# Kernel optimization log

Hardware: AMD Instinct MI355X
Metric: run time of the kernel (lower is better)

## Reference

```python
import jax, jax.numpy as jnp
import numpy as np
from jax import lax

EPS = 1e-5

def _conv(x, w, pad):
    # x: NCHW, w: OIHW, stride 1
    return lax.conv_general_dilated(x, w, (1, 1), [(pad, pad), (pad, pad)],
                                    dimension_numbers=('NCHW', 'OIHW', 'NCHW'))

def _binconv(x, w):
    # IR-Net/ReActNet HardBinaryConv: sign-binarized weights scaled by per-filter
    # mean |w| (alpha), sign-binarized activations; clip-based STE for backward.
    alpha = jnp.mean(jnp.abs(w), axis=(1, 2, 3), keepdims=True)  # [O,1,1,1]
    wc = jnp.clip(w, -1.0, 1.0)
    bw = lax.stop_gradient(alpha * jnp.sign(w) - wc) + wc
    xc = jnp.clip(x, -1.0, 1.0)
    ba = lax.stop_gradient(jnp.sign(x) - xc) + xc
    return _conv(ba, bw, 1)

def _bn(x, g, b, m, v):
    # inference-mode BatchNorm2d with running stats
    inv = g / jnp.sqrt(v + EPS)
    return x * inv[None, :, None, None] + (b - m * inv)[None, :, None, None]

def _pool(x):
    return lax.reduce_window(x, -jnp.inf, lax.max, (1, 1, 2, 2), (1, 1, 2, 2), 'VALID')

def _htanh(x):
    return jnp.clip(x, -1.0, 1.0)

def setup_inputs() -> dict:
    key = jax.random.key(0)
    ks = jax.random.split(key, 40)
    B = 256
    d = {'x': jax.random.normal(ks[0], (B, 3, 32, 32), jnp.float32)}
    shapes = [(128, 3, 3, 3), (128, 128, 3, 3), (256, 128, 3, 3),
              (256, 256, 3, 3), (512, 256, 3, 3), (512, 512, 3, 3)]
    chans = [128, 128, 256, 256, 512, 512]
    ki = 1
    for i, (ws, c) in enumerate(zip(shapes, chans)):
        fan_in = ws[1] * 9
        d[f'w{i}'] = jax.random.normal(ks[ki], ws, jnp.float32) / np.sqrt(fan_in); ki += 1
        d[f'g{i}'] = jnp.ones((c,), jnp.float32)
        d[f'b{i}'] = jnp.zeros((c,), jnp.float32)
        d[f'm{i}'] = jax.random.normal(ks[ki], (c,), jnp.float32) * 0.1; ki += 1
        d[f'v{i}'] = jax.random.uniform(ks[ki], (c,), jnp.float32, 0.5, 1.5); ki += 1
    d['fcw'] = jax.random.normal(ks[ki], (10, 512 * 4 * 4), jnp.float32) * 0.01
    d['fcb'] = jnp.zeros((10,), jnp.float32)
    return d

def reference(x, w0, g0, b0, m0, v0, w1, g1, b1, m1, v1, w2, g2, b2, m2, v2,
              w3, g3, b3, m3, v3, w4, g4, b4, m4, v4, w5, g5, b5, m5, v5,
              fcw, fcb):
    h = _bn(_conv(x, w0, 1), g0, b0, m0, v0)            # [B,128,32,32]
    h = _htanh(_bn(_pool(_binconv(h, w1)), g1, b1, m1, v1))   # [B,128,16,16]
    h = _htanh(_bn(_binconv(h, w2), g2, b2, m2, v2))          # [B,256,16,16]
    h = _htanh(_bn(_pool(_binconv(h, w3)), g3, b3, m3, v3))   # [B,256,8,8]
    h = _htanh(_bn(_binconv(h, w4), g4, b4, m4, v4))          # [B,512,8,8]
    h = _htanh(_bn(_pool(_binconv(h, w5)), g5, b5, m5, v5))   # [B,512,4,4]
    h = h.reshape(h.shape[0], -1)                             # [B,8192]
    return h @ fcw.T + fcb                                    # [B,10]
```

## Files before the change

kernel.cpp:

```cpp
#include <hip/hip_runtime.h>
#include <cstdint>

#define EPS 1e-5
typedef unsigned long long u64;
typedef unsigned int u32;

struct BnArgs { const float *g[6], *b[6], *m[6], *v[6]; };
struct PackArgs { const float* w[5]; u64* wb[5]; };

__global__ void bn_prep_all(BnArgs p, double* __restrict__ scale_all,
                            double* __restrict__ shift_all) {
    int i = blockIdx.x * 256 + threadIdx.x;
    if (i >= 1792) return;
    int l, base;
    if (i < 128)       { l = 0; base = 0; }
    else if (i < 256)  { l = 1; base = 128; }
    else if (i < 512)  { l = 2; base = 256; }
    else if (i < 768)  { l = 3; base = 512; }
    else if (i < 1280) { l = 4; base = 768; }
    else               { l = 5; base = 1280; }
    const int c = i - base;
    double inv = (double)p.g[l][c] / sqrt((double)p.v[l][c] + EPS);
    scale_all[i] = inv;
    shift_all[i] = (double)p.b[l][c] - (double)p.m[l][c] * inv;
}

__global__ void zero_out(float* __restrict__ out, int n) {
    int i = blockIdx.x * blockDim.x + threadIdx.x;
    if (i < n) out[i] = 0.f;
}

__global__ void pack_all(PackArgs pk, const double* __restrict__ scale_all,
                         double* __restrict__ A_all) {
    const int ob = blockIdx.x;
    const int t = threadIdx.x;
    int l, base, Cin, bnoff;
    if (ob < 128)       { l = 0; base = 0;    Cin = 128; bnoff = 128; }
    else if (ob < 384)  { l = 1; base = 128;  Cin = 128; bnoff = 256; }
    else if (ob < 640)  { l = 2; base = 384;  Cin = 256; bnoff = 512; }
    else if (ob < 1152) { l = 3; base = 640;  Cin = 256; bnoff = 768; }
    else                { l = 4; base = 1152; Cin = 512; bnoff = 1280; }
    const int o = ob - base;
    const float* wo = pk.w[l] + (size_t)o * Cin * 9;

    double s = 0.0;
    for (int k = t; k < Cin * 9; k += 256) s += fabs((double)wo[k]);
    __shared__ double red[256];
    red[t] = s;
    __syncthreads();
    for (int r = 128; r > 0; r >>= 1) {
        if (t < r) red[t] += red[t + r];
        __syncthreads();
    }
    if (t == 0) {
        double alpha = red[0] / (double)(Cin * 9);
        A_all[ob] = alpha * scale_all[bnoff + o];
    }

    const int W64 = Cin / 64;
    u64* wb = pk.wb[l];
    for (int e = t; e < 9 * W64; e += 256) {
        int tap = e / W64, word = e % W64;
        u64 bits = 0;
        for (int j = 0; j < 64; ++j) {
            int c = word * 64 + j;
            if (wo[c * 9 + tap] < 0.f) bits |= (1ull << j);
        }
        wb[((size_t)o * 9 + tap) * W64 + word] = bits;
    }
}

__global__ __launch_bounds__(256) void conv0_pack(
        const float* __restrict__ x, const float* __restrict__ w0,
        const double* __restrict__ scale, const double* __restrict__ shift,
        u64* __restrict__ bits0) {
    __shared__ double wlds[128 * 27];
    __shared__ double sc[128], sh[128];
    const int tid = threadIdx.x;
    for (int e = tid; e < 128 * 27; e += 256) wlds[e] = (double)w0[e];
    for (int e = tid; e < 128; e += 256) { sc[e] = scale[e]; sh[e] = shift[e]; }
    __syncthreads();

    const int n = blockIdx.y;
    const int p = blockIdx.x * 256 + tid;
    const int y = p >> 5, xx = p & 31;
    const float* xn = x + (size_t)n * 3 * 32 * 32;

    double win[27];
#pragma unroll
    for (int c = 0; c < 3; ++c)
#pragma unroll
        for (int dy = 0; dy < 3; ++dy)
#pragma unroll
            for (int dx = 0; dx < 3; ++dx) {
                const int yy = y + dy - 1, xs = xx + dx - 1;
                const bool ok = (yy >= 0 && yy < 32 && xs >= 0 && xs < 32);
                win[(c * 3 + dy) * 3 + dx] = ok ? (double)xn[(c * 32 + yy) * 32 + xs] : 0.0;
            }

    u64* op = bits0 + ((size_t)n * 1024 + p) * 2;
#pragma unroll
    for (int og = 0; og < 2; ++og) {
        u64 word = 0;
#pragma unroll 2
        for (int j = 0; j < 64; ++j) {
            const int o = og * 64 + j;
            const double* wo = &wlds[o * 27];
            double acc = 0.0;
#pragma unroll
            for (int k = 0; k < 27; ++k) acc = fma(wo[k], win[k], acc);
            const double val = acc * sc[o] + sh[o];
            word |= (u64)(val < 0.0) << j;
        }
        op[og] = word;
    }
}

template<int H, int W, int W64, int OTOT, int OPW, int MINW>
__global__ __launch_bounds__(256, MINW) void bconv_np(
        const u64* __restrict__ in_bits, const u64* __restrict__ wb,
        const double* __restrict__ A, const double* __restrict__ B,
        u32* __restrict__ out_bits) {
    const int tid = threadIdx.x;
    const int wave = tid >> 6, lane = tid & 63;
    constexpr int WPI = (H * W) / 64;
    constexpr int IPB = (WPI >= 4) ? 1 : 4 / WPI;
    const int img = (IPB == 1) ? blockIdx.y : blockIdx.y * IPB + wave;
    const int pw  = (IPB == 1) ? wave : 0;
    const int p = pw * 64 + lane;
    const int y = p / W, x = p % W;
    const int obase = blockIdx.x * OPW;

    __shared__ u64 wlds[OPW * 9 * W64];
    __shared__ double Alds[OPW], Blds[OPW];
    {
        const u64* wg = wb + (size_t)obase * 9 * W64;
        for (int e = tid; e < OPW * 9 * W64; e += 256) wlds[e] = wg[e];
        for (int e = tid; e < OPW; e += 256) { Alds[e] = A[obase + e]; Blds[e] = B[obase + e]; }
    }
    __syncthreads();

    const u64* ib = in_bits + (size_t)img * H * W * W64;
    u64 win[3][3][W64];
    bool tv[3][3];
    int nvalid = 0;
#pragma unroll
    for (int dy = 0; dy < 3; ++dy)
#pragma unroll
        for (int dx = 0; dx < 3; ++dx) {
            const int yy = y + dy - 1, xs = x + dx - 1;
            const bool ok = (yy >= 0 && yy < H && xs >= 0 && xs < W);
            tv[dy][dx] = ok;
            nvalid += ok ? 1 : 0;
            const u64* q = ib + ((size_t)yy * W + xs) * W64;
#pragma unroll
            for (int k = 0; k < W64; ++k) win[dy][dx][k] = ok ? q[k] : 0ull;
        }
    const int basev = nvalid * 64 * W64;

    u32 obuf[OPW / 32];
    u32 cur = 0;
    for (int oc = 0; oc < OPW; ++oc) {
        const u64* wo = &wlds[oc * 9 * W64];
        int pop = 0;
#pragma unroll
        for (int dy = 0; dy < 3; ++dy)
#pragma unroll
            for (int dx = 0; dx < 3; ++dx) {
                int tp = 0;
#pragma unroll
                for (int k = 0; k < W64; ++k)
                    tp += (int)__popcll(win[dy][dx][k] ^ wo[(dy * 3 + dx) * W64 + k]);
                pop += tv[dy][dx] ? tp : 0;
            }
        const int v = basev - 2 * pop;
        const double t = fma(Alds[oc], (double)v, Blds[oc]);
        cur |= (u32)(t < 0.0) << (oc & 31);
        if ((oc & 31) == 31) { obuf[oc >> 5] = cur; cur = 0; }
    }
    u32* op = out_bits + ((size_t)img * H * W + (size_t)y * W + x) * (OTOT / 32) + (obase >> 5);
#pragma unroll
    for (int j = 0; j < OPW / 32; ++j) op[j] = obuf[j];
}

template<int H, int W, int W64, int OTOT, int OPW, int MINW, bool LAST>
__global__ __launch_bounds__(256, MINW) void bconv_ps(
        const u64* __restrict__ in_bits, const u64* __restrict__ wb,
        const double* __restrict__ A, const double* __restrict__ B,
        u32* __restrict__ out_bits, float* __restrict__ h5) {
    const int tid = threadIdx.x;
    const int wave = tid >> 6, lane = tid & 63;
    constexpr int RPW = 64 / W;
    constexpr int WPI = (H * W) / 64;
    constexpr int IPB = (WPI >= 4) ? 1 : 4 / WPI;
    const int img = (IPB == 1) ? blockIdx.z : blockIdx.z * IPB + wave;
    const int wii = (IPB == 1) ? blockIdx.y * 4 + wave : 0;
    const int y = wii * RPW + lane / W;
    const int x = lane % W;
    const int obase = blockIdx.x * OPW;
    constexpr int Hp = H / 2, Wp = W / 2;

    __shared__ u64 wlds[OPW * 9 * W64];
    __shared__ double Alds[OPW], Blds[OPW];
    {
        const u64* wg = wb + (size_t)obase * 9 * W64;
        for (int e = tid; e < OPW * 9 * W64; e += 256) wlds[e] = wg[e];
        for (int e = tid; e < OPW; e += 256) { Alds[e] = A[obase + e]; Blds[e] = B[obase + e]; }
    }
    __syncthreads();

    const u64* ib = in_bits + (size_t)img * H * W * W64;
    u64 win[3][3][W64];
    bool tv[3][3];
    int nvalid = 0;
#pragma unroll
    for (int dy = 0; dy < 3; ++dy)
#pragma unroll
        for (int dx = 0; dx < 3; ++dx) {
            const int yy = y + dy - 1, xs = x + dx - 1;
            const bool ok = (yy >= 0 && yy < H && xs >= 0 && xs < W);
            tv[dy][dx] = ok;
            nvalid += ok ? 1 : 0;
            const u64* q = ib + ((size_t)yy * W + xs) * W64;
#pragma unroll
            for (int k = 0; k < W64; ++k) win[dy][dx][k] = ok ? q[k] : 0ull;
        }
    const int basev = nvalid * 64 * W64;
    const bool writer = ((lane & 1) == 0) && ((lane & W) == 0);
    const int py = y >> 1, px = x >> 1;

    u32 obuf[OPW / 32];
    u32 cur = 0;
    for (int oc = 0; oc < OPW; ++oc) {
        const u64* wo = &wlds[oc * 9 * W64];
        int pop = 0;
#pragma unroll
        for (int dy = 0; dy < 3; ++dy)
#pragma unroll
            for (int dx = 0; dx < 3; ++dx) {
                int tp = 0;
#pragma unroll
                for (int k = 0; k < W64; ++k)
                    tp += (int)__popcll(win[dy][dx][k] ^ wo[(dy * 3 + dx) * W64 + k]);
                pop += tv[dy][dx] ? tp : 0;
            }
        const int v = basev - 2 * pop;
        int v2 = max(v, __shfl_xor(v, 1, 64));
        int v4 = max(v2, __shfl_xor(v2, W, 64));
        if (LAST) {
            const double t = fma(Alds[oc], (double)v4, Blds[oc]);
            const double hcl = fmin(1.0, fmax(-1.0, t));
            if (writer)
                h5[(((size_t)img * OTOT + obase + oc) * Hp + py) * Wp + px] = (float)hcl;
        } else {
            const double t = fma(Alds[oc], (double)v4, Blds[oc]);
            cur |= (u32)(t < 0.0) << (oc & 31);
            if ((oc & 31) == 31) { obuf[oc >> 5] = cur; cur = 0; }
        }
    }
    if (!LAST && writer) {
        u32* op = out_bits + ((size_t)img * Hp * Wp + (size_t)py * Wp + px) * (OTOT / 32) + (obase >> 5);
#pragma unroll
        for (int j = 0; j < OPW / 32; ++j) op[j] = obuf[j];
    }
}

__global__ void fc_kernel(const float* __restrict__ h, const float* __restrict__ fcw,
                          const float* __restrict__ fcb, float* __restrict__ out) {
    const int n = blockIdx.x, t = threadIdx.x;
    double acc[10];
#pragma unroll
    for (int j = 0; j < 10; ++j) acc[j] = 0.0;
    const float* hn = h + (size_t)n * 8192;
    for (int k = t; k < 8192; k += 256) {
        double xv = (double)hn[k];
#pragma unroll
        for (int j = 0; j < 10; ++j) acc[j] += xv * (double)fcw[j * 8192 + k];
    }
    __shared__ double red[10][256];
#pragma unroll
    for (int j = 0; j < 10; ++j) red[j][t] = acc[j];
    __syncthreads();
    for (int r = 128; r > 0; r >>= 1) {
        if (t < r) {
#pragma unroll
            for (int j = 0; j < 10; ++j) red[j][t] += red[j][t + r];
        }
        __syncthreads();
    }
    if (t < 10) out[n * 10 + t] = (float)(red[t][0] + (double)fcb[t]);
}

extern "C" void kernel_launch(void* const* d_in, const int* in_sizes, int n_in,
                              void* d_out, int out_size, void* d_ws, size_t ws_size,
                              hipStream_t stream) {
    const float* X = (const float*)d_in[0];
    BnArgs bn;
    PackArgs pk;
    const float* Wt0 = (const float*)d_in[1];
    for (int i = 0; i < 6; ++i) {
        bn.g[i] = (const float*)d_in[2 + 5 * i];
        bn.b[i] = (const float*)d_in[3 + 5 * i];
        bn.m[i] = (const float*)d_in[4 + 5 * i];
        bn.v[i] = (const float*)d_in[5 + 5 * i];
    }
    for (int i = 0; i < 5; ++i) pk.w[i] = (const float*)d_in[1 + 5 * (i + 1)];
    const float* fcw = (const float*)d_in[31];
    const float* fcb = (const float*)d_in[32];
    float* out = (float*)d_out;

    char* ws = (char*)d_ws;
    size_t off = 0;
    auto alloc = [&](size_t bytes) -> void* {
        void* p = ws + off;
        off = (off + bytes + 255) & ~(size_t)255;
        return p;
    };

    double* scale_all = (double*)alloc(1792 * sizeof(double));
    double* shift_all = (double*)alloc(1792 * sizeof(double));
    double* A_all     = (double*)alloc(1664 * sizeof(double));
    const size_t WBN[5] = {128ull * 9 * 2, 256ull * 9 * 2, 256ull * 9 * 4,
                           512ull * 9 * 4, 512ull * 9 * 8};
    for (int i = 0; i < 5; ++i) pk.wb[i] = (u64*)alloc(WBN[i] * sizeof(u64));
    u64* bits0 = (u64*)alloc(256ull * 32 * 32 * 2 * sizeof(u64));
    u64* bits1 = (u64*)alloc(256ull * 16 * 16 * 2 * sizeof(u64));
    u64* bits2 = (u64*)alloc(256ull * 16 * 16 * 4 * sizeof(u64));
    u64* bits3 = (u64*)alloc(256ull * 8 * 8 * 4 * sizeof(u64));
    u64* bits4 = (u64*)alloc(256ull * 8 * 8 * 8 * sizeof(u64));
    float* h5  = (float*)alloc(256ull * 8192 * sizeof(float));

    if (off > ws_size) {
        zero_out<<<dim3((out_size + 255) / 256), dim3(256), 0, stream>>>(out, out_size);
        return;
    }

    const int BOF[6] = {0, 128, 256, 512, 768, 1280};
    const int AOF[5] = {0, 128, 384, 640, 1152};

    bn_prep_all<<<dim3(7), dim3(256), 0, stream>>>(bn, scale_all, shift_all);
    pack_all<<<dim3(1664), dim3(256), 0, stream>>>(pk, scale_all, A_all);

    conv0_pack<<<dim3(4, 256), dim3(256), 0, stream>>>(
        X, Wt0, scale_all + BOF[0], shift_all + BOF[0], bits0);

    bconv_ps<32, 32, 2, 128, 64, 4, false><<<dim3(2, 4, 256), dim3(256), 0, stream>>>(
        bits0, pk.wb[0], A_all + AOF[0], shift_all + BOF[1], (u32*)bits1, nullptr);
    bconv_np<16, 16, 2, 256, 64, 4><<<dim3(4, 256), dim3(256), 0, stream>>>(
        bits1, pk.wb[1], A_all + AOF[1], shift_all + BOF[2], (u32*)bits2);
    bconv_ps<16, 16, 4, 256, 32, 3, false><<<dim3(8, 1, 256), dim3(256), 0, stream>>>(
        bits2, pk.wb[2], A_all + AOF[2], shift_all + BOF[3], (u32*)bits3, nullptr);
    bconv_np<8, 8, 4, 512, 32, 3><<<dim3(16, 64), dim3(256), 0, stream>>>(
        bits3, pk.wb[3], A_all + AOF[3], shift_all + BOF[4], (u32*)bits4);
    bconv_ps<8, 8, 8, 512, 32, 2, true><<<dim3(16, 1, 64), dim3(256), 0, stream>>>(
        bits4, pk.wb[4], A_all + AOF[4], shift_all + BOF[5], nullptr, h5);

    fc_kernel<<<dim3(256), dim3(256), 0, stream>>>(h5, fcw, fcb, out);
}
```

Before: 608.6 us.

## Restructure binary convs to tap-major loop with per-channel register accumulators

Merges the pooled and non-pooled binary conv kernels into one template. The loop order changes to taps outer and output channels inner, keeping 32 popcount accumulators in registers. Weights are stored tap-major so each tap's slice for the block is contiguous, and they are read straight from global memory (wave-uniform, scalar-cacheable) instead of being staged in LDS. This removes the LDS staging, the barrier and the large per-thread window array, but every block now re-reads weights from cache, and the two 32x32 and 16x16 layers move from 64 to 32 output channels per block, doubling the number of blocks.

```diff
diff --git a/kernel.cpp b/kernel.cpp
--- a/kernel.cpp
+++ b/kernel.cpp
@@ -6,7 +6,7 @@
 typedef unsigned int u32;
 
 struct BnArgs { const float *g[6], *b[6], *m[6], *v[6]; };
-struct PackArgs { const float* w[5]; u64* wb[5]; };
+struct PackArgs { const float* w[5]; u64* wbt[5]; };
 
 __global__ void bn_prep_all(BnArgs p, double* __restrict__ scale_all,
                             double* __restrict__ shift_all) {
@@ -34,12 +34,12 @@
                          double* __restrict__ A_all) {
     const int ob = blockIdx.x;
     const int t = threadIdx.x;
-    int l, base, Cin, bnoff;
-    if (ob < 128)       { l = 0; base = 0;    Cin = 128; bnoff = 128; }
-    else if (ob < 384)  { l = 1; base = 128;  Cin = 128; bnoff = 256; }
-    else if (ob < 640)  { l = 2; base = 384;  Cin = 256; bnoff = 512; }
-    else if (ob < 1152) { l = 3; base = 640;  Cin = 256; bnoff = 768; }
-    else                { l = 4; base = 1152; Cin = 512; bnoff = 1280; }
+    int l, base, Cin, bnoff, OTOT;
+    if (ob < 128)       { l = 0; base = 0;    Cin = 128; bnoff = 128;  OTOT = 128; }
+    else if (ob < 384)  { l = 1; base = 128;  Cin = 128; bnoff = 256;  OTOT = 256; }
+    else if (ob < 640)  { l = 2; base = 384;  Cin = 256; bnoff = 512;  OTOT = 256; }
+    else if (ob < 1152) { l = 3; base = 640;  Cin = 256; bnoff = 768;  OTOT = 512; }
+    else                { l = 4; base = 1152; Cin = 512; bnoff = 1280; OTOT = 512; }
     const int o = ob - base;
     const float* wo = pk.w[l] + (size_t)o * Cin * 9;
 
@@ -58,7 +58,7 @@
     }
 
     const int W64 = Cin / 64;
-    u64* wb = pk.wb[l];
+    u64* wbt = pk.wbt[l];
     for (int e = t; e < 9 * W64; e += 256) {
         int tap = e / W64, word = e % W64;
         u64 bits = 0;
@@ -66,7 +66,7 @@
             int c = word * 64 + j;
             if (wo[c * 9 + tap] < 0.f) bits |= (1ull << j);
         }
-        wb[((size_t)o * 9 + tap) * W64 + word] = bits;
+        wbt[((size_t)tap * OTOT + o) * W64 + word] = bits;
     }
 }
 
@@ -116,152 +116,76 @@
     }
 }
 
-template<int H, int W, int W64, int OTOT, int OPW, int MINW>
-__global__ __launch_bounds__(256, MINW) void bconv_np(
-        const u64* __restrict__ in_bits, const u64* __restrict__ wb,
-        const double* __restrict__ A, const double* __restrict__ B,
-        u32* __restrict__ out_bits) {
-    const int tid = threadIdx.x;
-    const int wave = tid >> 6, lane = tid & 63;
-    constexpr int WPI = (H * W) / 64;
-    constexpr int IPB = (WPI >= 4) ? 1 : 4 / WPI;
-    const int img = (IPB == 1) ? blockIdx.y : blockIdx.y * IPB + wave;
-    const int pw  = (IPB == 1) ? wave : 0;
-    const int p = pw * 64 + lane;
-    const int y = p / W, x = p % W;
-    const int obase = blockIdx.x * OPW;
-
-    __shared__ u64 wlds[OPW * 9 * W64];
-    __shared__ double Alds[OPW], Blds[OPW];
-    {
-        const u64* wg = wb + (size_t)obase * 9 * W64;
-        for (int e = tid; e < OPW * 9 * W64; e += 256) wlds[e] = wg[e];
-        for (int e = tid; e < OPW; e += 256) { Alds[e] = A[obase + e]; Blds[e] = B[obase + e]; }
-    }
-    __syncthreads();
-
-    const u64* ib = in_bits + (size_t)img * H * W * W64;
-    u64 win[3][3][W64];
-    bool tv[3][3];
-    int nvalid = 0;
-#pragma unroll
-    for (int dy = 0; dy < 3; ++dy)
-#pragma unroll
-        for (int dx = 0; dx < 3; ++dx) {
-            const int yy = y + dy - 1, xs = x + dx - 1;
-            const bool ok = (yy >= 0 && yy < H && xs >= 0 && xs < W);
-            tv[dy][dx] = ok;
-            nvalid += ok ? 1 : 0;
-            const u64* q = ib + ((size_t)yy * W + xs) * W64;
-#pragma unroll
-            for (int k = 0; k < W64; ++k) win[dy][dx][k] = ok ? q[k] : 0ull;
-        }
-    const int basev = nvalid * 64 * W64;
-
-    u32 obuf[OPW / 32];
-    u32 cur = 0;
-    for (int oc = 0; oc < OPW; ++oc) {
-        const u64* wo = &wlds[oc * 9 * W64];
-        int pop = 0;
-#pragma unroll
-        for (int dy = 0; dy < 3; ++dy)
-#pragma unroll
-            for (int dx = 0; dx < 3; ++dx) {
-                int tp = 0;
-#pragma unroll
-                for (int k = 0; k < W64; ++k)
-                    tp += (int)__popcll(win[dy][dx][k] ^ wo[(dy * 3 + dx) * W64 + k]);
-                pop += tv[dy][dx] ? tp : 0;
-            }
-        const int v = basev - 2 * pop;
-        const double t = fma(Alds[oc], (double)v, Blds[oc]);
-        cur |= (u32)(t < 0.0) << (oc & 31);
-        if ((oc & 31) == 31) { obuf[oc >> 5] = cur; cur = 0; }
-    }
-    u32* op = out_bits + ((size_t)img * H * W + (size_t)y * W + x) * (OTOT / 32) + (obase >> 5);
-#pragma unroll
-    for (int j = 0; j < OPW / 32; ++j) op[j] = obuf[j];
-}
-
-template<int H, int W, int W64, int OTOT, int OPW, int MINW, bool LAST>
-__global__ __launch_bounds__(256, MINW) void bconv_ps(
-        const u64* __restrict__ in_bits, const u64* __restrict__ wb,
+template<int H, int W, int W64, int OTOT, bool POOL, bool LAST, int MINW>
+__global__ __launch_bounds__(256, MINW) void bconv3(
+        const u64* __restrict__ in_bits, const u64* __restrict__ wbt,
         const double* __restrict__ A, const double* __restrict__ B,
         u32* __restrict__ out_bits, float* __restrict__ h5) {
     const int tid = threadIdx.x;
     const int wave = tid >> 6, lane = tid & 63;
-    constexpr int RPW = 64 / W;
+    constexpr int OPW = 32;
     constexpr int WPI = (H * W) / 64;
-    constexpr int IPB = (WPI >= 4) ? 1 : 4 / WPI;
+    constexpr int IPB = (WPI >= 4) ? 1 : (4 / WPI);
     const int img = (IPB == 1) ? blockIdx.z : blockIdx.z * IPB + wave;
-    const int wii = (IPB == 1) ? blockIdx.y * 4 + wave : 0;
-    const int y = wii * RPW + lane / W;
+    const int wii = (IPB == 1) ? (blockIdx.y * 4 + wave) : 0;
+    const int y = wii * (64 / W) + lane / W;
     const int x = lane % W;
     const int obase = blockIdx.x * OPW;
-    constexpr int Hp = H / 2, Wp = W / 2;
-
-    __shared__ u64 wlds[OPW * 9 * W64];
-    __shared__ double Alds[OPW], Blds[OPW];
-    {
-        const u64* wg = wb + (size_t)obase * 9 * W64;
-        for (int e = tid; e < OPW * 9 * W64; e += 256) wlds[e] = wg[e];
-        for (int e = tid; e < OPW; e += 256) { Alds[e] = A[obase + e]; Blds[e] = B[obase + e]; }
-    }
-    __syncthreads();
 
     const u64* ib = in_bits + (size_t)img * H * W * W64;
-    u64 win[3][3][W64];
-    bool tv[3][3];
+
+    int acc[OPW];
+#pragma unroll
+    for (int i = 0; i < OPW; ++i) acc[i] = 0;
     int nvalid = 0;
-#pragma unroll
-    for (int dy = 0; dy < 3; ++dy)
-#pragma unroll
+
+#pragma unroll 1
+    for (int dy = 0; dy < 3; ++dy) {
+#pragma unroll 1
         for (int dx = 0; dx < 3; ++dx) {
             const int yy = y + dy - 1, xs = x + dx - 1;
             const bool ok = (yy >= 0 && yy < H && xs >= 0 && xs < W);
-            tv[dy][dx] = ok;
             nvalid += ok ? 1 : 0;
+            u64 wn[W64];
             const u64* q = ib + ((size_t)yy * W + xs) * W64;
 #pragma unroll
-            for (int k = 0; k < W64; ++k) win[dy][dx][k] = ok ? q[k] : 0ull;
-        }
+            for (int k = 0; k < W64; ++k) wn[k] = ok ? q[k] : 0ull;
+            const u64* wt = wbt + ((size_t)(dy * 3 + dx) * OTOT + obase) * W64;
+#pragma unroll
+            for (int oc = 0; oc < OPW; ++oc) {
+                int tp = 0;
+#pragma unroll
+                for (int k = 0; k < W64; ++k)
+                    tp += (int)__popcll(wn[k] ^ wt[oc * W64 + k]);
+                acc[oc] += ok ? tp : 0;
+            }
+        }
+    }
+
     const int basev = nvalid * 64 * W64;
-    const bool writer = ((lane & 1) == 0) && ((lane & W) == 0);
-    const int py = y >> 1, px = x >> 1;
-
-    u32 obuf[OPW / 32];
+    constexpr int Hp = POOL ? H / 2 : H, Wp = POOL ? W / 2 : W;
+    const bool writer = (!POOL) || (((lane & 1) == 0) && ((lane & W) == 0));
+    const int py = POOL ? (y >> 1) : y, px = POOL ? (x >> 1) : x;
+
     u32 cur = 0;
+#pragma unroll
     for (int oc = 0; oc < OPW; ++oc) {
-        const u64* wo = &wlds[oc * 9 * W64];
-        int pop = 0;
-#pragma unroll
-        for (int dy = 0; dy < 3; ++dy)
-#pragma unroll
-            for (int dx = 0; dx < 3; ++dx) {
-                int tp = 0;
-#pragma unroll
-                for (int k = 0; k < W64; ++k)
-                    tp += (int)__popcll(win[dy][dx][k] ^ wo[(dy * 3 + dx) * W64 + k]);
-                pop += tv[dy][dx] ? tp : 0;
-            }
-        const int v = basev - 2 * pop;
-        int v2 = max(v, __shfl_xor(v, 1, 64));
-        int v4 = max(v2, __shfl_xor(v2, W, 64));
+        int v = basev - 2 * acc[oc];
+        if (POOL) {
+            int v2 = max(v, __shfl_xor(v, 1, 64));
+            v = max(v2, __shfl_xor(v2, W, 64));
+        }
+        const double t = fma(A[obase + oc], (double)v, B[obase + oc]);
         if (LAST) {
-            const double t = fma(Alds[oc], (double)v4, Blds[oc]);
             const double hcl = fmin(1.0, fmax(-1.0, t));
             if (writer)
                 h5[(((size_t)img * OTOT + obase + oc) * Hp + py) * Wp + px] = (float)hcl;
         } else {
-            const double t = fma(Alds[oc], (double)v4, Blds[oc]);
-            cur |= (u32)(t < 0.0) << (oc & 31);
-            if ((oc & 31) == 31) { obuf[oc >> 5] = cur; cur = 0; }
+            cur |= (u32)(t < 0.0) << oc;
         }
     }
     if (!LAST && writer) {
-        u32* op = out_bits + ((size_t)img * Hp * Wp + (size_t)py * Wp + px) * (OTOT / 32) + (obase >> 5);
-#pragma unroll
-        for (int j = 0; j < OPW / 32; ++j) op[j] = obuf[j];
+        out_bits[((size_t)img * Hp * Wp + (size_t)py * Wp + px) * (OTOT / 32) + (obase >> 5)] = cur;
     }
 }
 
@@ -322,7 +246,7 @@
     double* A_all     = (double*)alloc(1664 * sizeof(double));
     const size_t WBN[5] = {128ull * 9 * 2, 256ull * 9 * 2, 256ull * 9 * 4,
                            512ull * 9 * 4, 512ull * 9 * 8};
-    for (int i = 0; i < 5; ++i) pk.wb[i] = (u64*)alloc(WBN[i] * sizeof(u64));
+    for (int i = 0; i < 5; ++i) pk.wbt[i] = (u64*)alloc(WBN[i] * sizeof(u64));
     u64* bits0 = (u64*)alloc(256ull * 32 * 32 * 2 * sizeof(u64));
     u64* bits1 = (u64*)alloc(256ull * 16 * 16 * 2 * sizeof(u64));
     u64* bits2 = (u64*)alloc(256ull * 16 * 16 * 4 * sizeof(u64));
@@ -344,16 +268,16 @@
     conv0_pack<<<dim3(4, 256), dim3(256), 0, stream>>>(
         X, Wt0, scale_all + BOF[0], shift_all + BOF[0], bits0);
 
-    bconv_ps<32, 32, 2, 128, 64, 4, false><<<dim3(2, 4, 256), dim3(256), 0, stream>>>(
-        bits0, pk.wb[0], A_all + AOF[0], shift_all + BOF[1], (u32*)bits1, nullptr);
-    bconv_np<16, 16, 2, 256, 64, 4><<<dim3(4, 256), dim3(256), 0, stream>>>(
-        bits1, pk.wb[1], A_all + AOF[1], shift_all + BOF[2], (u32*)bits2);
-    bconv_ps<16, 16, 4, 256, 32, 3, false><<<dim3(8, 1, 256), dim3(256), 0, stream>>>(
-        bits2, pk.wb[2], A_all + AOF[2], shift_all + BOF[3], (u32*)bits3, nullptr);
-    bconv_np<8, 8, 4, 512, 32, 3><<<dim3(16, 64), dim3(256), 0, stream>>>(
-        bits3, pk.wb[3], A_all + AOF[3], shift_all + BOF[4], (u32*)bits4);
-    bconv_ps<8, 8, 8, 512, 32, 2, true><<<dim3(16, 1, 64), dim3(256), 0, stream>>>(
-        bits4, pk.wb[4], A_all + AOF[4], shift_all + BOF[5], nullptr, h5);
+    bconv3<32, 32, 2, 128, true, false, 4><<<dim3(4, 4, 256), dim3(256), 0, stream>>>(
+        bits0, pk.wbt[0], A_all + AOF[0], shift_all + BOF[1], (u32*)bits1, nullptr);
+    bconv3<16, 16, 2, 256, false, false, 4><<<dim3(8, 1, 256), dim3(256), 0, stream>>>(
+        bits1, pk.wbt[1], A_all + AOF[1], shift_all + BOF[2], (u32*)bits2, nullptr);
+    bconv3<16, 16, 4, 256, true, false, 4><<<dim3(8, 1, 256), dim3(256), 0, stream>>>(
+        bits2, pk.wbt[2], A_all + AOF[2], shift_all + BOF[3], (u32*)bits3, nullptr);
+    bconv3<8, 8, 4, 512, false, false, 4><<<dim3(16, 1, 64), dim3(256), 0, stream>>>(
+        bits3, pk.wbt[3], A_all + AOF[3], shift_all + BOF[4], (u32*)bits4, nullptr);
+    bconv3<8, 8, 8, 512, true, true, 4><<<dim3(16, 1, 64), dim3(256), 0, stream>>>(
+        bits4, pk.wbt[4], A_all + AOF[4], shift_all + BOF[5], nullptr, h5);
 
     fc_kernel<<<dim3(256), dim3(256), 0, stream>>>(h5, fcw, fcb, out);
 }
```

After: 593.6 us. 1.03x faster.
